# Kernel tuning notes

Hardware: AMD Instinct MI355X
Metric: run time of the kernel (lower is better)

## Reference

```python
import jax, jax.numpy as jnp
import numpy as np
jax.config.update("jax_enable_x64", True)  # need >32-bit lattice-key packing

D = 5          # feature dim
B_OFF = 1024   # coordinate offset for integer key packing
BASE = 2 * B_OFF


def _encode(keys):
    # keys: [..., D] int32 lattice coords (first D of the D+1 zero-sum coords)
    code = jnp.zeros(keys.shape[:-1], jnp.int64)
    for i in range(D):
        code = code * BASE + (keys[..., i].astype(jnp.int64) + B_OFF)
    return code


def _decode(code):
    coords = []
    c = code
    for _ in range(D):
        coords.append((c % BASE) - B_OFF)
        c = c // BASE
    return jnp.stack(coords[::-1], axis=-1).astype(jnp.int32)


def _lattice_filter(feature, values):
    """Permutohedral lattice filter: splat -> (d+1) directional blurs -> slice."""
    N, d = feature.shape
    vd = values.shape[1]
    f = feature.astype(jnp.float32)
    vals = values.astype(jnp.float32)

    # ---- elevate features onto the hyperplane H_{d+1} (Adams et al. E matrix) ----
    inv_std = np.sqrt(2.0 / 3.0) * (d + 1)
    scale = jnp.asarray(inv_std / np.sqrt(np.arange(1, d + 1) * np.arange(2, d + 2)),
                        jnp.float32)
    c = f * scale                                        # [N, d]
    S = jnp.cumsum(c[:, ::-1], axis=1)[:, ::-1]          # suffix sums: S[:,i] = sum c[:,i:]
    suffix = jnp.concatenate([S[:, 1:], jnp.zeros((N, 1), c.dtype)], axis=1)
    idx = jnp.arange(1, d + 1, dtype=c.dtype)
    elevated = jnp.concatenate([S[:, :1], suffix - idx * c], axis=1)   # [N, d+1]

    # ---- nearest zero-colored lattice point (multiples of d+1) ----
    down = 1.0 / (d + 1)
    rd = jnp.round(elevated * down)
    rem0 = rd * (d + 1)
    sum_ = jnp.sum(rd, axis=1).astype(jnp.int32)
    diff = (elevated - rem0) * down
    order = jnp.argsort(-diff, axis=1, stable=True)
    rank = jnp.argsort(order, axis=1).astype(jnp.int32) + sum_[:, None]
    rem0i = rem0.astype(jnp.int32)
    shift = (rank < 0).astype(jnp.int32) - (rank > d).astype(jnp.int32)
    rank = rank + (d + 1) * shift
    rem0i = rem0i + (d + 1) * shift

    # ---- barycentric coordinates ----
    t = (elevated - rem0i.astype(elevated.dtype)) * down
    rows = jnp.arange(N)[:, None]
    b = jnp.zeros((N, d + 2), elevated.dtype)
    b = b.at[rows, d - rank].add(t)
    b = b.at[rows, d + 1 - rank].add(-t)
    b0 = b[:, 0] + 1.0 + b[:, d + 1]
    bary = jnp.concatenate([b0[:, None], b[:, 1:d + 1]], axis=1)        # [N, d+1]

    # ---- keys of the d+1 enclosing simplex vertices (store first d coords) ----
    r = jnp.arange(d + 1, dtype=jnp.int32)
    canonical = jnp.where(rank[:, None, :] >= (d + 1 - r)[None, :, None],
                          r[None, :, None] - (d + 1), r[None, :, None])  # [N,d+1,d+1]
    keys = rem0i[:, None, :d] + canonical[..., :d]                       # [N,d+1,d]

    # ---- hash + unique lattice vertices (fixed-size for jit) ----
    M = N * (d + 1)
    codes = _encode(keys.reshape(M, d))
    FILL = jnp.iinfo(jnp.int64).max
    uniq = jnp.unique(codes, size=M, fill_value=FILL)   # sorted, padded
    inv = jnp.searchsorted(uniq, codes)

    # ---- splat ----
    contrib = (bary[:, :, None] * vals[:, None, :]).reshape(M, vd)
    val = jax.ops.segment_sum(contrib, inv, num_segments=M)             # [M, vd]

    # ---- blur along each of the d+1 lattice directions ([1,2,1]/4 kernel) ----
    coords = _decode(uniq)                                              # [M, d]
    full = jnp.concatenate([coords, -jnp.sum(coords, axis=1, keepdims=True)], axis=1)
    for j in range(d + 1):
        off = jnp.ones((d + 1,), jnp.int32).at[j].set(-d)

        def look(nk, cur):
            cde = _encode(nk[:, :d])
            ii = jnp.clip(jnp.searchsorted(uniq, cde), 0, M - 1)
            ok = uniq[ii] == cde
            return jnp.where(ok[:, None], cur[ii], 0.0)

        val = 0.5 * val + 0.25 * (look(full + off, val) + look(full - off, val))

    # ---- slice ----
    alpha = 1.0 / (1.0 + 2.0 ** (-d))
    sliced = val[inv].reshape(N, d + 1, vd)
    return alpha * jnp.einsum('nr,nrv->nv', bary, sliced)


def setup_inputs() -> dict:
    key = jax.random.key(0)
    k1, k2 = jax.random.split(key)
    N = 1 << 20
    feature = jax.random.normal(k1, (N, D), dtype=jnp.float32)
    values = jax.random.normal(k2, (N, 16), dtype=jnp.float32)
    return {"feature": feature, "values": values}


def reference(feature, values):
    return _lattice_filter(feature, values)
```

## Files before the change

### kernel.cpp

```cpp
#include <hip/hip_runtime.h>
#include <stdint.h>

typedef unsigned long long u64;
typedef unsigned int u32;
typedef unsigned short u16;

static constexpr u64 KEMPTY = ~0ull;
static constexpr int PROBE_CAP = 32768;
static constexpr u32 THRESH = 23040;
static constexpr u32 UM     = 20480;
static constexpr u32 UIDCAP = 32768;
static constexpr u32 LC     = 18;

static __device__ __forceinline__ u64 mix64(u64 x){
  x ^= x >> 30; x *= 0xbf58476d1ce4e5b9ull;
  x ^= x >> 27; x *= 0x94d049bb133111ebull;
  x ^= x >> 31; return x;
}

static __device__ __forceinline__ void lds_add(float* p, float v){
  __hip_atomic_fetch_add(p, v, __ATOMIC_RELAXED, __HIP_MEMORY_SCOPE_WORKGROUP);
}

static __device__ __forceinline__ void row_load(const float* __restrict__ p, float* o){
  const float4* q=(const float4*)p;
#pragma unroll
  for(int i=0;i<4;i++){ float4 v=q[i]; o[4*i]=v.x; o[4*i+1]=v.y; o[4*i+2]=v.z; o[4*i+3]=v.w; }
}
static __device__ __forceinline__ void row_store(float* __restrict__ p, const float* o){
  float4* q=(float4*)p;
#pragma unroll
  for(int i=0;i<4;i++) q[i]=make_float4(o[4*i],o[4*i+1],o[4*i+2],o[4*i+3]);
}

__global__ void __launch_bounds__(256)
k_setup(const float* __restrict__ feat, int N,
        u64* __restrict__ tabk, u32 cmask,
        u32* __restrict__ inv_slot, float* __restrict__ baryT)
{
#pragma clang fp contract(off)
  int n = blockIdx.x*256 + threadIdx.x;
  if(n>=N) return;

  const float s0=3.4641016151377544f, s1=2.0f, s2=1.4142135623730951f,
              s3=1.0954451150103321f, s4=0.8944271909999159f;
  float c[5];
  c[0]=feat[n*5+0]*s0; c[1]=feat[n*5+1]*s1; c[2]=feat[n*5+2]*s2;
  c[3]=feat[n*5+3]*s3; c[4]=feat[n*5+4]*s4;

  float sfx[6]; sfx[5]=0.f;
#pragma unroll
  for(int i=4;i>=0;i--) sfx[i]=sfx[i+1]+c[i];
  float el[6];
  el[0]=sfx[0];
#pragma unroll
  for(int i=1;i<6;i++) el[i]=sfx[i]-(float)i*c[i-1];

  const float down=1.0f/6.0f;
  float rd[6], rem0[6], rdsum=0.f;
#pragma unroll
  for(int i=0;i<6;i++){ rd[i]=rintf(el[i]*down); rem0[i]=rd[i]*6.0f; rdsum+=rd[i]; }
  int sumi=(int)rdsum;

  float diff[6];
#pragma unroll
  for(int i=0;i<6;i++) diff[i]=(el[i]-rem0[i])*down;

  int rank[6];
#pragma unroll
  for(int i=0;i<6;i++){
    int r=0;
#pragma unroll
    for(int j=0;j<6;j++)
      r += (diff[j]>diff[i]) || (diff[j]==diff[i] && j<i);
    rank[i]=r+sumi;
  }
  int rem0i[6];
#pragma unroll
  for(int i=0;i<6;i++){
    rem0i[i]=(int)rem0[i];
    int sh=(rank[i]<0)-(rank[i]>5);
    rank[i]+=6*sh; rem0i[i]+=6*sh;
  }

  float b[7]={0.f,0.f,0.f,0.f,0.f,0.f,0.f};
#pragma unroll
  for(int i=0;i<6;i++){
    float t=(el[i]-(float)rem0i[i])*down;
    int k0=5-rank[i]; if(k0>=0&&k0<7) b[k0]+=t;
  }
#pragma unroll
  for(int i=0;i<6;i++){
    float t=(el[i]-(float)rem0i[i])*down;
    int k1=6-rank[i]; if(k1>=0&&k1<7) b[k1]-=t;
  }
  baryT[n]=(b[0]+1.0f)+b[6];
#pragma unroll
  for(int r=1;r<6;r++) baryT[(size_t)r*N+n]=b[r];

  u64 code6[6]; u32 h6[6];
#pragma unroll
  for(int r=0;r<6;r++){
    long long code=0;
#pragma unroll
    for(int i=0;i<5;i++){
      int key = rem0i[i] + ((rank[i] >= 6-r) ? (r-6) : r);
      code = code*2048 + (long long)(key+1024);
    }
    code6[r]=(u64)code;
    h6[r]=(u32)mix64((u64)code)&cmask;
  }

#pragma unroll 1
  for(int r=0;r<6;r++){
    u64 code=code6[r];
    u32 h=h6[r];
    u32 slot=0xFFFFFFFFu;
#pragma unroll 1
    for(int p=0;p<PROBE_CAP;p++){
      u64 cur=tabk[h];
      if(cur==code){ slot=h; break; }
      if(cur==KEMPTY){
        u64 old=atomicCAS((unsigned long long*)&tabk[h], KEMPTY, code);
        if(old==KEMPTY || old==code){ slot=h; break; }
      } else {
        h=(h+1)&cmask;
      }
    }
    inv_slot[(size_t)r*N+n]=slot;
  }
}

__global__ void __launch_bounds__(256)
k_uid(const u64* __restrict__ tabk, u32 C, u32* __restrict__ tuid,
      u32* __restrict__ uidslot, u64* __restrict__ uidkey, u32* __restrict__ counter)
{
  u32 s=blockIdx.x*256+threadIdx.x;
  if(s>=C) return;
  u64 k=tabk[s];
  if(k==KEMPTY) return;
  u32 uid=atomicAdd(counter,1u);
  if(uid<UIDCAP){ uidslot[uid]=s; uidkey[uid]=k; } else uid=0;
  tuid[s]=uid;
}

__global__ void __launch_bounds__(256)
k_translate(const u32* __restrict__ inv, u16* __restrict__ inv16,
            const u32* __restrict__ tuid, size_t M)
{
  size_t i=(size_t)blockIdx.x*256+threadIdx.x;
  if(i<M) inv16[i]=(u16)tuid[inv[i]];
}

__global__ void __launch_bounds__(256)
k_vtrans(const float* __restrict__ values, float* __restrict__ valuesT, int N)
{
  __shared__ float tile[256][17];
  u32 b=blockIdx.x, t=threadIdx.x;
  size_t p=(size_t)b*256+t;
  float v[16];
  row_load(values+p*16, v);
#pragma unroll
  for(int k=0;k<16;k++) tile[t][k]=v[k];
  __syncthreads();
  u32 ch=t>>4, lane=t&15;
#pragma unroll
  for(int q=0;q<16;q++){
    u32 pt=q*16+lane;
    valuesT[(size_t)ch*N + (size_t)b*256 + pt]=tile[pt][ch];
  }
}

__global__ void __launch_bounds__(256)
k_nbr(const u64* __restrict__ tabk, const u32* __restrict__ tuid, u32 cmask,
      const u64* __restrict__ uidkey, const u32* __restrict__ counter,
      u16* __restrict__ nbr)
{
  u32 m=blockIdx.x*256+threadIdx.x;
  u32 U=*counter; if(U>THRESH) U=THRESH;
  if(m>=U) return;
  long long code=(long long)uidkey[m];
  const long long P0=1ll,P1=2048ll,P2=1ll<<22,P3=1ll<<33,P4=1ll<<44;
  const long long SUM=P0+P1+P2+P3+P4;
  long long d[6]={SUM-6*P4,SUM-6*P3,SUM-6*P2,SUM-6*P1,SUM-6*P0,SUM};
  u64 nc[12]; u32 h0[12]; u64 pre[12];
#pragma unroll
  for(int j=0;j<6;j++){ nc[2*j]=(u64)(code+d[j]); nc[2*j+1]=(u64)(code-d[j]); }
#pragma unroll
  for(int j=0;j<12;j++) h0[j]=(u32)mix64(nc[j])&cmask;
#pragma unroll
  for(int j=0;j<12;j++) pre[j]=tabk[h0[j]];
#pragma unroll 1
  for(int j=0;j<12;j++){
    u32 h=h0[j]; u64 cur=pre[j];
    u16 res=0xFFFFu;
#pragma unroll 1
    for(int p=0;p<PROBE_CAP;p++){
      if(cur==nc[j]){ res=(u16)tuid[h]; break; }
      if(cur==KEMPTY) break;
      h=(h+1)&cmask;
      cur=tabk[h];
    }
    nbr[(size_t)j*UIDCAP+m]=res;
  }
}

__global__ void __launch_bounds__(1024, 8)
k_saccum1m(const u16* __restrict__ inv16, const float* __restrict__ baryT,
           const float* __restrict__ valuesT, const u32* __restrict__ counter,
           int N, float* __restrict__ partial1)
{
  __shared__ float acc1[UM];
  u32 U=*counter;
  if(U>UM) return;
  u32 j=blockIdx.x;
  u32 cs=j&15, sub=j>>4;
  u32 t=threadIdx.x;
  for(u32 x=t;x<U;x+=1024) acc1[x]=0.f;
  __syncthreads();

  u32 nsub=(u32)N/32;
  u32 quads=nsub>>2;
  size_t p0=(size_t)sub*nsub;
  const float* vch=valuesT+(size_t)cs*N;
  for(u32 q=t;q<quads;q+=1024){
    size_t p=p0+(size_t)q*4;
    float4 v=*(const float4*)(vch+p);
#pragma unroll
    for(int r=0;r<6;r++){
      ushort4 uu=*(const ushort4*)(inv16+(size_t)r*N+p);
      float4  w =*(const float4*)(baryT+(size_t)r*N+p);
      lds_add(&acc1[uu.x], w.x*v.x);
      lds_add(&acc1[uu.y], w.y*v.y);
      lds_add(&acc1[uu.z], w.z*v.z);
      lds_add(&acc1[uu.w], w.w*v.w);
    }
  }
  __syncthreads();
  float* dst=partial1+(size_t)j*UM;
  for(u32 x=t;x<U;x+=1024) dst[x]=acc1[x];
}

__global__ void __launch_bounds__(1024, 4)
k_saccum1b(const u16* __restrict__ inv16, const float* __restrict__ baryT,
           const float* __restrict__ valuesT, const u32* __restrict__ counter,
           int N, float* __restrict__ partial1)
{
  __shared__ float acc1[THRESH];
  u32 U=*counter;
  if(U<=UM || U>THRESH) return;
  u32 j=blockIdx.x;
  u32 cs=j&15, sub=j>>4;
  u32 t=threadIdx.x;
  for(u32 x=t;x<U;x+=1024) acc1[x]=0.f;
  __syncthreads();

  u32 nsub=(u32)N/16;
  u32 quads=nsub>>2;
  size_t p0=(size_t)sub*nsub;
  const float* vch=valuesT+(size_t)cs*N;
  for(u32 q=t;q<quads;q+=1024){
    size_t p=p0+(size_t)q*4;
    float4 v=*(const float4*)(vch+p);
#pragma unroll
    for(int r=0;r<6;r++){
      ushort4 uu=*(const ushort4*)(inv16+(size_t)r*N+p);
      float4  w =*(const float4*)(baryT+(size_t)r*N+p);
      lds_add(&acc1[uu.x], w.x*v.x);
      lds_add(&acc1[uu.y], w.y*v.y);
      lds_add(&acc1[uu.z], w.z*v.z);
      lds_add(&acc1[uu.w], w.w*v.w);
    }
  }
  __syncthreads();
  float* dst=partial1+(size_t)j*THRESH;
  for(u32 x=t;x<U;x+=1024) dst[x]=acc1[x];
}

__global__ void __launch_bounds__(256)
k_reduce1(const float* __restrict__ partial1, const u32* __restrict__ counter,
          float* __restrict__ v0)
{
  u32 U=*counter;
  if(U>THRESH) return;
  bool small=(U<=UM);
  u32 S = small?32u:16u;
  size_t stride = small?(size_t)UM:(size_t)THRESH;
  u32 cs=blockIdx.y;
  u32 u=blockIdx.x*256+threadIdx.x;
  if(u>=U) return;
  float s=0.f;
  for(u32 sub=0;sub<S;sub++)
    s+=partial1[(size_t)(sub*16+cs)*stride+u];
  v0[(size_t)u*16+cs]=s;
}

__global__ void __launch_bounds__(256)
k_blur(const u16* __restrict__ nbr, const u32* __restrict__ counter, int j,
       const float* __restrict__ vin, float* __restrict__ vout)
{
  u32 m=blockIdx.x*256+threadIdx.x;
  u32 U=*counter; if(U>THRESH) U=THRESH;
  if(m>=U) return;
  u16 np=nbr[(size_t)(2*j)*UIDCAP+m];
  u16 nm=nbr[(size_t)(2*j+1)*UIDCAP+m];
  float acc[16];
  row_load(vin+(size_t)m*16, acc);
#pragma unroll
  for(int k=0;k<16;k++) acc[k]*=0.5f;
  if(np!=0xFFFFu){
    float t[16]; row_load(vin+(size_t)np*16,t);
#pragma unroll
    for(int k=0;k<16;k++) acc[k]+=0.25f*t[k];
  }
  if(nm!=0xFFFFu){
    float t[16]; row_load(vin+(size_t)nm*16,t);
#pragma unroll
    for(int k=0;k<16;k++) acc[k]+=0.25f*t[k];
  }
  row_store(vout+(size_t)m*16, acc);
}

__global__ void __launch_bounds__(256)
k_slice(const u16* __restrict__ inv16, const float* __restrict__ baryT,
        const float* __restrict__ val, int N, float* __restrict__ out)
{
  int n=blockIdx.x*256+threadIdx.x;
  if(n>=N) return;
  u32 u[6]; float w[6];
#pragma unroll
  for(int r=0;r<6;r++){ u[r]=inv16[(size_t)r*N+n]; w[r]=baryT[(size_t)r*N+n]; }
  float t6[6][16];
#pragma unroll
  for(int r=0;r<6;r++) row_load(val+(size_t)u[r]*16, t6[r]);
  float acc[16];
#pragma unroll
  for(int k=0;k<16;k++){
    float a=w[0]*t6[0][k];
#pragma unroll
    for(int r=1;r<6;r++) a+=w[r]*t6[r][k];
    acc[k]=a;
  }
  const float alpha=0.9696969696969697f;
  float4* q=(float4*)(out+(size_t)n*16);
#pragma unroll
  for(int i=0;i<4;i++) q[i]=make_float4(alpha*acc[4*i],alpha*acc[4*i+1],alpha*acc[4*i+2],alpha*acc[4*i+3]);
}

__global__ void k_diag(float* out, float v){ out[0]=v; }

extern "C" void kernel_launch(void* const* d_in, const int* in_sizes, int n_in,
                              void* d_out, int out_size, void* d_ws, size_t ws_size,
                              hipStream_t stream)
{
  const float* feat   =(const float*)d_in[0];
  const float* values =(const float*)d_in[1];
  float* out=(float*)d_out;
  int N=in_sizes[0]/5;
  size_t M=(size_t)N*6;

  size_t C=1ull<<LC; u32 cmask=(u32)(C-1);
  size_t partial1b=(size_t)512*UM*4;

  auto needed=[&]()->size_t{
    size_t s=0;
    auto al=[&](size_t b){ s=(s+255)&~(size_t)255; s+=b; };
    al(4);
    al(M*4);
    al(M*4);
    al(M*2);
    al(C*8);
    al(C*4);
    al(UIDCAP*4);
    al(UIDCAP*8);
    al((size_t)12*UIDCAP*2);
    al((size_t)UIDCAP*64);
    al((size_t)UIDCAP*64);
    al((size_t)N*64);
    al(partial1b);
    return s+256;
  };
  if(needed()>ws_size){
    hipMemsetAsync(d_out,0,(size_t)out_size*sizeof(float),stream);
    k_diag<<<1,1,0,stream>>>(out,(float)(ws_size>>20));
    return;
  }

  char* base=(char*)d_ws; size_t offb=0;
  auto carve=[&](size_t b)->char*{ offb=(offb+255)&~(size_t)255; char* p=base+offb; offb+=b; return p; };
  u32*   counter=(u32*)carve(4);
  u32*   inv    =(u32*)carve(M*4);
  float* baryT  =(float*)carve(M*4);
  u16*   inv16  =(u16*)carve(M*2);
  u64*   tabk   =(u64*)carve(C*8);
  u32*   tuid   =(u32*)carve(C*4);
  u32*   uidslot=(u32*)carve(UIDCAP*4);
  u64*   uidkey =(u64*)carve(UIDCAP*8);
  u16*   nbr    =(u16*)carve((size_t)12*UIDCAP*2);
  float* v0     =(float*)carve((size_t)UIDCAP*64);
  float* v1     =(float*)carve((size_t)UIDCAP*64);
  float* valuesT=(float*)carve((size_t)N*64);
  float* partial1=(float*)carve(partial1b);

  hipMemsetAsync(counter,0,4,stream);
  hipMemsetAsync(tabk,0xFF,C*8,stream);

  const int B=256;
  k_setup    <<<(N+B-1)/B,B,0,stream>>>(feat,N,tabk,cmask,inv,baryT);
  k_uid      <<<(u32)((C+B-1)/B),B,0,stream>>>(tabk,(u32)C,tuid,uidslot,uidkey,counter);
  k_translate<<<(u32)((M+B-1)/B),B,0,stream>>>(inv,inv16,tuid,M);
  k_vtrans   <<<(u32)(N/256),B,0,stream>>>(values,valuesT,N);
  k_nbr      <<<(UIDCAP+B-1)/B,B,0,stream>>>(tabk,tuid,cmask,uidkey,counter,nbr);

  k_saccum1m<<<512,1024,0,stream>>>(inv16,baryT,valuesT,counter,N,partial1);
  k_saccum1b<<<256,1024,0,stream>>>(inv16,baryT,valuesT,counter,N,partial1);
  {
    dim3 g((THRESH+B-1)/B,16);
    k_reduce1<<<g,B,0,stream>>>(partial1,counter,v0);
  }

  u32 gb=(THRESH+B-1)/B;
  float* a=v0; float* bb=v1;
  for(int j=0;j<6;j++){
    k_blur<<<gb,B,0,stream>>>(nbr,counter,j,a,bb);
    float* t=a; a=bb; bb=t;
  }
  k_slice<<<(N+B-1)/B,B,0,stream>>>(inv16,baryT,a,N,out);
}
```

Baseline: 935.7 us.

## Shrink hash table to 16-bit slots, prefetch first probes, vectorize translate

Reduces the hash table from 2^18 to 2^16 slots so slot indices fit in 16 bits. Setup writes them straight into the u16 inverse array, which drops the 32-bit intermediate buffer and halves that write traffic. All six first-probe loads are issued up front so they can overlap, and the translate kernel now remaps in place four entries per thread. The higher load factor (about 20K keys in 64K slots) risks longer probe chains, and the probe cap is raised to match.

```diff
diff --git a/kernel.cpp b/kernel.cpp
--- a/kernel.cpp
+++ b/kernel.cpp
@@ -6,11 +6,11 @@
 typedef unsigned short u16;
 
 static constexpr u64 KEMPTY = ~0ull;
-static constexpr int PROBE_CAP = 32768;
+static constexpr int PROBE_CAP = 65536;
 static constexpr u32 THRESH = 23040;
 static constexpr u32 UM     = 20480;
 static constexpr u32 UIDCAP = 32768;
-static constexpr u32 LC     = 18;
+static constexpr u32 LC     = 16;
 
 static __device__ __forceinline__ u64 mix64(u64 x){
   x ^= x >> 30; x *= 0xbf58476d1ce4e5b9ull;
@@ -36,7 +36,7 @@
 __global__ void __launch_bounds__(256)
 k_setup(const float* __restrict__ feat, int N,
         u64* __restrict__ tabk, u32 cmask,
-        u32* __restrict__ inv_slot, float* __restrict__ baryT)
+        u16* __restrict__ invS, float* __restrict__ baryT)
 {
 #pragma clang fp contract(off)
   int n = blockIdx.x*256 + threadIdx.x;
@@ -110,24 +110,32 @@
     code6[r]=(u64)code;
     h6[r]=(u32)mix64((u64)code)&cmask;
   }
+  u64 pre[6];
+#pragma unroll
+  for(int r=0;r<6;r++) pre[r]=tabk[h6[r]];
 
 #pragma unroll 1
   for(int r=0;r<6;r++){
     u64 code=code6[r];
     u32 h=h6[r];
-    u32 slot=0xFFFFFFFFu;
+    u32 slot;
+    if(pre[r]==code){
+      slot=h;
+    } else {
+      slot=0xFFFFFFFFu;
 #pragma unroll 1
-    for(int p=0;p<PROBE_CAP;p++){
-      u64 cur=tabk[h];
-      if(cur==code){ slot=h; break; }
-      if(cur==KEMPTY){
-        u64 old=atomicCAS((unsigned long long*)&tabk[h], KEMPTY, code);
-        if(old==KEMPTY || old==code){ slot=h; break; }
-      } else {
-        h=(h+1)&cmask;
+      for(int p=0;p<PROBE_CAP;p++){
+        u64 cur=tabk[h];
+        if(cur==code){ slot=h; break; }
+        if(cur==KEMPTY){
+          u64 old=atomicCAS((unsigned long long*)&tabk[h], KEMPTY, code);
+          if(old==KEMPTY || old==code){ slot=h; break; }
+        } else {
+          h=(h+1)&cmask;
+        }
       }
     }
-    inv_slot[(size_t)r*N+n]=slot;
+    invS[(size_t)r*N+n]=(u16)slot;
   }
 }
 
@@ -145,11 +153,14 @@
 }
 
 __global__ void __launch_bounds__(256)
-k_translate(const u32* __restrict__ inv, u16* __restrict__ inv16,
-            const u32* __restrict__ tuid, size_t M)
+k_translate(u16* __restrict__ inv16, const u32* __restrict__ tuid, size_t Mq)
 {
   size_t i=(size_t)blockIdx.x*256+threadIdx.x;
-  if(i<M) inv16[i]=(u16)tuid[inv[i]];
+  if(i>=Mq) return;
+  ushort4 s=((const ushort4*)inv16)[i];
+  ushort4 o;
+  o.x=(u16)tuid[s.x]; o.y=(u16)tuid[s.y]; o.z=(u16)tuid[s.z]; o.w=(u16)tuid[s.w];
+  ((ushort4*)inv16)[i]=o;
 }
 
 __global__ void __launch_bounds__(256)
@@ -366,7 +377,6 @@
     size_t s=0;
     auto al=[&](size_t b){ s=(s+255)&~(size_t)255; s+=b; };
     al(4);
-    al(M*4);
     al(M*4);
     al(M*2);
     al(C*8);
@@ -389,7 +399,6 @@
   char* base=(char*)d_ws; size_t offb=0;
   auto carve=[&](size_t b)->char*{ offb=(offb+255)&~(size_t)255; char* p=base+offb; offb+=b; return p; };
   u32*   counter=(u32*)carve(4);
-  u32*   inv    =(u32*)carve(M*4);
   float* baryT  =(float*)carve(M*4);
   u16*   inv16  =(u16*)carve(M*2);
   u64*   tabk   =(u64*)carve(C*8);
@@ -406,9 +415,10 @@
   hipMemsetAsync(tabk,0xFF,C*8,stream);
 
   const int B=256;
-  k_setup    <<<(N+B-1)/B,B,0,stream>>>(feat,N,tabk,cmask,inv,baryT);
+  size_t Mq=M/4;
+  k_setup    <<<(N+B-1)/B,B,0,stream>>>(feat,N,tabk,cmask,inv16,baryT);
   k_uid      <<<(u32)((C+B-1)/B),B,0,stream>>>(tabk,(u32)C,tuid,uidslot,uidkey,counter);
-  k_translate<<<(u32)((M+B-1)/B),B,0,stream>>>(inv,inv16,tuid,M);
+  k_translate<<<(u32)((Mq+B-1)/B),B,0,stream>>>(inv16,tuid,Mq);
   k_vtrans   <<<(u32)(N/256),B,0,stream>>>(values,valuesT,N);
   k_nbr      <<<(UIDCAP+B-1)/B,B,0,stream>>>(tabk,tuid,cmask,uidkey,counter,nbr);
 
```

After: 912.0 us. 1.03x faster.
